# Performance work log

Hardware: AMD Instinct MI355X
Metric: run time of the kernel (lower is better)

Reference implementation:

```python
import jax, jax.numpy as jnp
from jax import lax
import numpy as np
import math

B, T, D = 4, 4096, 1024
K, H = 128, 8
KH = K // H
KER = 4
M = 4 * D  # mlp hidden


def _ln(x, g, b):
    m = jnp.mean(x, axis=-1, keepdims=True)
    v = jnp.var(x, axis=-1, keepdims=True)
    return (x - m) / jnp.sqrt(v + 1e-5) * g + b


def setup_inputs() -> dict:
    key = jax.random.key(0)
    ks = jax.random.split(key, 20)
    s = lambda i, shape, sc=0.02: jax.random.normal(ks[i], shape, dtype=jnp.float32) * sc
    inp = {}
    inp["x"] = jax.random.normal(ks[0], (B, T, D), dtype=jnp.float32)
    inp["prev_eig"] = jax.random.normal(ks[1], (B, T, 2 * K), dtype=jnp.float32)
    inp["in_proj_w"] = s(2, (2 * K, D))
    inp["conv_w"] = s(3, (2 * K, 1, KER), 0.3)          # depthwise Conv1d weight
    inp["conv_b"] = s(4, (2 * K,), 0.02)
    inp["mem_gate"] = jnp.float32(-3.0)
    inp["mem_proj_w"] = jnp.eye(2 * K, dtype=jnp.float32) + s(5, (2 * K, 2 * K), 0.02)
    # log_decay uniform in [center-1, center+0.5], center = -2 + 1.5*(1/5)
    center = -2.0 + 1.5 * (1.0 / 5.0)
    inp["log_decay"] = jax.random.uniform(ks[6], (K,), dtype=jnp.float32, minval=center - 1.0, maxval=center + 0.5)
    inp["frequency"] = jnp.linspace(0.0, 2.0 * math.pi * (1.0 - 1.0 / K), K, dtype=jnp.float32)
    inp["coupling"] = jnp.eye(KH, dtype=jnp.float32)[None] + 0.01 * jax.random.normal(ks[7], (H, KH, KH), dtype=jnp.float32) / math.sqrt(KH)
    inp["out_proj_w"] = s(8, (D, 2 * K))
    inp["gate_w"] = s(9, (D, D))
    inp["gate_b"] = jnp.full((D,), -2.0, dtype=jnp.float32)
    inp["mlp_w1"] = s(10, (M, D))
    inp["mlp_b1"] = jnp.zeros((M,), jnp.float32)
    inp["mlp_w2"] = s(11, (D, M))
    inp["mlp_b2"] = jnp.zeros((D,), jnp.float32)
    inp["n1_g"] = jnp.ones((D,), jnp.float32)
    inp["n1_b"] = jnp.zeros((D,), jnp.float32)
    inp["n2_g"] = jnp.ones((D,), jnp.float32)
    inp["n2_b"] = jnp.zeros((D,), jnp.float32)
    return inp


def reference(x, prev_eig, in_proj_w, conv_w, conv_b, mem_gate, mem_proj_w,
              log_decay, frequency, coupling, out_proj_w, gate_w, gate_b,
              mlp_w1, mlp_b1, mlp_w2, mlp_b2, n1_g, n1_b, n2_g, n2_b):
    Bn, Tn, Dn = x.shape
    xn = _ln(x, n1_g, n1_b)
    beta = xn @ in_proj_w.T                                   # [B,T,2K]
    # depthwise causal conv: torch pad=ker-1 both sides then [:, :, :T] == left-pad ker-1 + valid
    ker = conv_w.shape[-1]
    bp = jnp.pad(beta, ((0, 0), (ker - 1, 0), (0, 0))).transpose(0, 2, 1)  # [B,2K,T+ker-1]
    beta = lax.conv_general_dilated(bp, conv_w, (1,), 'VALID',
                                    feature_group_count=conv_w.shape[0],
                                    dimension_numbers=('NCH', 'OIH', 'NCH'))
    beta = jax.nn.silu(beta.transpose(0, 2, 1) + conv_b)       # [B,T,2K]
    br, bi = jnp.split(beta, 2, axis=-1)                       # [B,T,K] each
    # memory injection (has_memory: layer_idx > 0)
    mg = jax.nn.sigmoid(mem_gate)
    pr, pi = jnp.split(prev_eig @ mem_proj_w.T, 2, axis=-1)
    br = br + mg * pr
    bi = bi + mg * pi
    # eigenstate evolution via zero-padded complex FFT convolution
    mag = jax.nn.sigmoid(log_decay)                            # [K]
    n = jnp.arange(Tn, dtype=x.dtype)
    mag_pow = mag[None, :] ** n[:, None]                       # [T,K]
    phase = n[:, None] * frequency[None, :]
    kern = mag_pow * (jnp.cos(phase) + 1j * jnp.sin(phase))    # complex [T,K]
    beta_c = br + 1j * bi
    Bf = jnp.fft.fft(jnp.pad(beta_c, ((0, 0), (0, Tn), (0, 0))), axis=1)  # [B,2T,K]
    Kf = jnp.fft.fft(jnp.pad(kern, ((0, Tn), (0, 0))), axis=0)            # [2T,K]
    c = jnp.fft.ifft(Bf * Kf[None], axis=1)[:, :Tn]
    cr, ci = c.real.astype(x.dtype), c.imag.astype(x.dtype)
    # per-head coupling, batched over heads
    Hh, Kh = coupling.shape[0], coupling.shape[1]
    cr = jnp.einsum('hjk,bthk->bthj', coupling, cr.reshape(Bn, Tn, Hh, Kh)).reshape(Bn, Tn, Hh * Kh)
    ci = jnp.einsum('hjk,bthk->bthj', coupling, ci.reshape(Bn, Tn, Hh, Kh)).reshape(Bn, Tn, Hh * Kh)
    eig = jnp.concatenate([cr, ci], axis=-1)                   # [B,T,2K]
    h = jax.nn.sigmoid(xn @ gate_w.T + gate_b) * (eig @ out_proj_w.T)
    x1 = x + h
    y = _ln(x1, n2_g, n2_b)
    x2 = x1 + jax.nn.silu(y @ mlp_w1.T + mlp_b1) @ mlp_w2.T + mlp_b2
    return (x2, eig)
```

## Files before the change

### kernel.cpp

```cpp
#include <hip/hip_runtime.h>
#include <hip/hip_bf16.h>
#include <math.h>

#define Bn 4
#define Tn 4096
#define Dn 1024
#define Kn 128
#define TWOK 256
#define Hn 8
#define Mmlp 4096
#define NROW (Bn * Tn)
#define TAPS 16

typedef __attribute__((ext_vector_type(8))) short bf16x8;
typedef __attribute__((ext_vector_type(4))) float floatx4;

__device__ __forceinline__ float sigmoidf_(float x) { return 1.f / (1.f + expf(-x)); }

__global__ __launch_bounds__(256) void f2bf_kernel(const float* __restrict__ in,
                                                   __hip_bfloat16* __restrict__ out,
                                                   int n) {
    const int i = (blockIdx.x * 256 + threadIdx.x) * 4;
    if (i >= n) return;
    const float4 v = *(const float4*)(in + i);
    out[i + 0] = __float2bfloat16(v.x);
    out[i + 1] = __float2bfloat16(v.y);
    out[i + 2] = __float2bfloat16(v.z);
    out[i + 3] = __float2bfloat16(v.w);
}

__global__ __launch_bounds__(256) void ln_kernel(const float* __restrict__ x,
                                                 const float* __restrict__ g,
                                                 const float* __restrict__ b,
                                                 __hip_bfloat16* __restrict__ out) {
    const int row = blockIdx.x;
    const float4* xr = (const float4*)(x + (size_t)row * Dn);
    float4 v = xr[threadIdx.x];
    float s = v.x + v.y + v.z + v.w;
    float ss = v.x * v.x + v.y * v.y + v.z * v.z + v.w * v.w;
    for (int off = 32; off; off >>= 1) {
        s += __shfl_down(s, off);
        ss += __shfl_down(ss, off);
    }
    __shared__ float rs[4], rss[4];
    const int wv = threadIdx.x >> 6, ln = threadIdx.x & 63;
    if (ln == 0) { rs[wv] = s; rss[wv] = ss; }
    __syncthreads();
    s = rs[0] + rs[1] + rs[2] + rs[3];
    ss = rss[0] + rss[1] + rss[2] + rss[3];
    const float mean = s * (1.f / Dn);
    const float var = ss * (1.f / Dn) - mean * mean;
    const float inv = rsqrtf(var + 1e-5f);
    const float4 gg = ((const float4*)g)[threadIdx.x];
    const float4 bb = ((const float4*)b)[threadIdx.x];
    __hip_bfloat16* op = out + (size_t)row * Dn + threadIdx.x * 4;
    op[0] = __float2bfloat16((v.x - mean) * inv * gg.x + bb.x);
    op[1] = __float2bfloat16((v.y - mean) * inv * gg.y + bb.y);
    op[2] = __float2bfloat16((v.z - mean) * inv * gg.z + bb.z);
    op[3] = __float2bfloat16((v.w - mean) * inv * gg.w + bb.w);
}

template <int EPI, typename CT>
__global__ __launch_bounds__(256, 4) void gemm_bf(const ushort* __restrict__ A,
                                                  const ushort* __restrict__ B,
                                                  CT* __restrict__ C,
                                                  int M, int N, int Kd,
                                                  const float* __restrict__ bias,
                                                  const float* __restrict__ aux1,
                                                  const __hip_bfloat16* __restrict__ aux2) {
    __shared__ ushort As[128 * 32];
    __shared__ ushort Bs[128 * 32];
    const int tid = threadIdx.x;
    const int m0 = blockIdx.y * 128, n0 = blockIdx.x * 128;
    const int wave = tid >> 6, lane = tid & 63;
    const int wm = wave >> 1, wn = wave & 1;
    const int mlane = lane & 15, quad = lane >> 4;

    floatx4 acc[4][4] = {};

    const ushort* Ap = A + (size_t)m0 * Kd;
    const ushort* Bp = B + (size_t)n0 * Kd;

    for (int k0 = 0; k0 < Kd; k0 += 32) {
#pragma unroll
        for (int q = 0; q < 2; ++q) {
            const int c = q * 256 + tid;
            const int row = c >> 2, kc = (c & 3) * 8;
            __builtin_amdgcn_global_load_lds(
                (const __attribute__((address_space(1))) void*)(Ap + (size_t)row * Kd + k0 + kc),
                (__attribute__((address_space(3))) void*)(As + c * 8), 16, 0, 0);
            __builtin_amdgcn_global_load_lds(
                (const __attribute__((address_space(1))) void*)(Bp + (size_t)row * Kd + k0 + kc),
                (__attribute__((address_space(3))) void*)(Bs + c * 8), 16, 0, 0);
        }
        __syncthreads();

        bf16x8 af[4], bfr[4];
#pragma unroll
        for (int t = 0; t < 4; ++t) {
            af[t]  = *(const bf16x8*)&As[(wm * 64 + t * 16 + mlane) * 32 + quad * 8];
            bfr[t] = *(const bf16x8*)&Bs[(wn * 64 + t * 16 + mlane) * 32 + quad * 8];
        }
#pragma unroll
        for (int i = 0; i < 4; ++i)
#pragma unroll
            for (int j = 0; j < 4; ++j)
                acc[i][j] = __builtin_amdgcn_mfma_f32_16x16x32_bf16(af[i], bfr[j], acc[i][j], 0, 0, 0);
        __syncthreads();
    }

    float s_pre = 0.f;
    if constexpr (EPI == 1) s_pre = sigmoidf_(bias[0]);

    const int cbase = n0 + wn * 64 + mlane;
#pragma unroll
    for (int i = 0; i < 4; ++i) {
#pragma unroll
        for (int r = 0; r < 4; ++r) {
            const int row = m0 + wm * 64 + i * 16 + quad * 4 + r;
            const size_t ro = (size_t)row * N;
#pragma unroll
            for (int j = 0; j < 4; ++j) {
                const int col = cbase + j * 16;
                const float a = acc[i][j][r];
                float o;
                if constexpr (EPI == 0) {
                    o = a;
                } else if constexpr (EPI == 1) {
                    o = s_pre * a;
                } else if constexpr (EPI == 2) {
                    o = aux1[ro + col] + sigmoidf_(a + bias[col]) * __bfloat162float(aux2[ro + col]);
                } else if constexpr (EPI == 3) {
                    const float t = a + bias[col];
                    o = t * sigmoidf_(t);
                } else {
                    o = a + bias[col] + aux1[ro + col];
                }
                if constexpr (__is_same(CT, float)) C[ro + col] = o;
                else                                C[ro + col] = __float2bfloat16(o);
            }
        }
    }
}

#define TCH 256
#define BROWS (TCH + TAPS + 2)
#define UROWS (TCH + TAPS - 1)

__global__ __launch_bounds__(256) void cfc_kernel(const float* __restrict__ beta,
                                                  const float* __restrict__ mgp,
                                                  const float* __restrict__ conv_w,
                                                  const float* __restrict__ conv_b,
                                                  const float* __restrict__ log_decay,
                                                  const float* __restrict__ freq,
                                                  const float* __restrict__ coup,
                                                  float* __restrict__ eig,
                                                  __hip_bfloat16* __restrict__ eig_bf) {
    const int b = blockIdx.z, h = blockIdx.y, t0 = blockIdx.x * TCH;
    const int tid = threadIdx.x;

    __shared__ float sbeta[BROWS * 32];
    __shared__ float su[UROWS * 33];
    __shared__ float str[16 * TAPS], sti[16 * TAPS];
    __shared__ float scoup[16 * 16];
    __shared__ float scw[32 * 4], scb[32];

    auto chan = [&](int cg) { return (cg < 16) ? (h * 16 + cg) : (128 + h * 16 + cg - 16); };

    for (int idx = tid; idx < BROWS * 32; idx += 256) {
        const int r = idx >> 5, cg = idx & 31;
        const int t = t0 - (TAPS + 2) + r;
        sbeta[idx] = (t >= 0) ? beta[((size_t)b * Tn + t) * TWOK + chan(cg)] : 0.f;
    }
    for (int idx = tid; idx < UROWS * 32; idx += 256) {
        const int r = idx >> 5, cg = idx & 31;
        const int t = t0 - (TAPS - 1) + r;
        su[r * 33 + cg] = (t >= 0) ? mgp[((size_t)b * Tn + t) * TWOK + chan(cg)] : 0.f;
    }
    if (tid < 128) scw[tid] = conv_w[chan(tid >> 2) * 4 + (tid & 3)];
    else if (tid < 160) scb[tid - 128] = conv_b[chan(tid - 128)];
    scoup[tid] = coup[h * 256 + tid];
    {
        const int k = tid >> 4, d = tid & (TAPS - 1);
        const float mag = sigmoidf_(log_decay[h * 16 + k]);
        const float f = freq[h * 16 + k];
        const float p = powf(mag, (float)d);
        str[k * TAPS + d] = p * cosf(d * f);
        sti[k * TAPS + d] = p * sinf(d * f);
    }
    __syncthreads();

    for (int idx = tid; idx < UROWS * 32; idx += 256) {
        const int r = idx >> 5, cg = idx & 31;
        const int rb = r + 3;
        float v = sbeta[(rb - 3) * 32 + cg] * scw[cg * 4 + 0] +
                  sbeta[(rb - 2) * 32 + cg] * scw[cg * 4 + 1] +
                  sbeta[(rb - 1) * 32 + cg] * scw[cg * 4 + 2] +
                  sbeta[(rb - 0) * 32 + cg] * scw[cg * 4 + 3] + scb[cg];
        v = v * sigmoidf_(v);
        su[r * 33 + cg] += v;
    }
    __syncthreads();

    const int ru = tid + (TAPS - 1);
    float orr[16], oii[16];
#pragma unroll
    for (int j = 0; j < 16; ++j) { orr[j] = 0.f; oii[j] = 0.f; }
#pragma unroll 4
    for (int k = 0; k < 16; ++k) {
        float accr = 0.f, acci = 0.f;
#pragma unroll
        for (int d = 0; d < TAPS; ++d) {
            const float ur = su[(ru - d) * 33 + k];
            const float ui = su[(ru - d) * 33 + 16 + k];
            const float lr = str[k * TAPS + d], li = sti[k * TAPS + d];
            accr += lr * ur - li * ui;
            acci += lr * ui + li * ur;
        }
#pragma unroll
        for (int j = 0; j < 16; ++j) {
            orr[j] += scoup[j * 16 + k] * accr;
            oii[j] += scoup[j * 16 + k] * acci;
        }
    }
    const size_t base = ((size_t)b * Tn + t0 + tid) * TWOK + h * 16;
    float4* er = (float4*)(eig + base);
    float4* ei = (float4*)(eig + base + Kn);
#pragma unroll
    for (int q = 0; q < 4; ++q) {
        er[q] = make_float4(orr[4 * q], orr[4 * q + 1], orr[4 * q + 2], orr[4 * q + 3]);
        ei[q] = make_float4(oii[4 * q], oii[4 * q + 1], oii[4 * q + 2], oii[4 * q + 3]);
    }
#pragma unroll
    for (int j = 0; j < 16; ++j) {
        eig_bf[base + j] = __float2bfloat16(orr[j]);
        eig_bf[base + Kn + j] = __float2bfloat16(oii[j]);
    }
}

extern "C" void kernel_launch(void* const* d_in, const int* in_sizes, int n_in,
                              void* d_out, int out_size, void* d_ws, size_t ws_size,
                              hipStream_t stream) {
    const float* x          = (const float*)d_in[0];
    const float* prev_eig   = (const float*)d_in[1];
    const float* in_proj_w  = (const float*)d_in[2];
    const float* conv_w     = (const float*)d_in[3];
    const float* conv_b     = (const float*)d_in[4];
    const float* mem_gate   = (const float*)d_in[5];
    const float* mem_proj_w = (const float*)d_in[6];
    const float* log_decay  = (const float*)d_in[7];
    const float* frequency  = (const float*)d_in[8];
    const float* coupling   = (const float*)d_in[9];
    const float* out_proj_w = (const float*)d_in[10];
    const float* gate_w     = (const float*)d_in[11];
    const float* gate_b     = (const float*)d_in[12];
    const float* mlp_w1     = (const float*)d_in[13];
    const float* mlp_b1     = (const float*)d_in[14];
    const float* mlp_w2     = (const float*)d_in[15];
    const float* mlp_b2     = (const float*)d_in[16];
    const float* n1_g       = (const float*)d_in[17];
    const float* n1_b       = (const float*)d_in[18];
    const float* n2_g       = (const float*)d_in[19];
    const float* n2_b       = (const float*)d_in[20];

    float* out = (float*)d_out;
    float* eig = out + (size_t)NROW * Dn;

    char* wsb = (char*)d_ws;
    const size_t MB = 1 << 20;
    float* x1    = (float*)(wsb + 0);
    float* beta  = (float*)(wsb + 0);
    float* mgp   = (float*)(wsb + 16 * MB);
    __hip_bfloat16* h1      = (__hip_bfloat16*)(wsb + 64 * MB);
    __hip_bfloat16* o_bf    = (__hip_bfloat16*)(wsb + 64 * MB);
    __hip_bfloat16* eig_bf  = (__hip_bfloat16*)(wsb + 96 * MB);
    __hip_bfloat16* peig_bf = (__hip_bfloat16*)(wsb + 104 * MB);
    __hip_bfloat16* xn_bf   = (__hip_bfloat16*)(wsb + 128 * MB);
    __hip_bfloat16* y_bf    = (__hip_bfloat16*)(wsb + 160 * MB);
    __hip_bfloat16* w1_bf   = (__hip_bfloat16*)(wsb + 192 * MB);
    __hip_bfloat16* w2_bf   = (__hip_bfloat16*)(wsb + 200 * MB);
    __hip_bfloat16* gate_bf = (__hip_bfloat16*)(wsb + 208 * MB);
    __hip_bfloat16* inpj_bf = (__hip_bfloat16*)(wsb + 210 * MB);
    __hip_bfloat16* outpj_bf= (__hip_bfloat16*)(wsb + 210 * MB + 512 * 1024);
    __hip_bfloat16* mempj_bf= (__hip_bfloat16*)(wsb + 211 * MB);

    auto cvt = [&](const float* src, __hip_bfloat16* dst, int n) {
        f2bf_kernel<<<dim3((n / 4 + 255) / 256), dim3(256), 0, stream>>>(src, dst, n);
    };
    cvt(in_proj_w,  inpj_bf,  TWOK * Dn);
    cvt(mem_proj_w, mempj_bf, TWOK * TWOK);
    cvt(out_proj_w, outpj_bf, Dn * TWOK);
    cvt(gate_w,     gate_bf,  Dn * Dn);
    cvt(mlp_w1,     w1_bf,    Mmlp * Dn);
    cvt(mlp_w2,     w2_bf,    Dn * Mmlp);
    cvt(prev_eig,   peig_bf,  NROW * TWOK);

    ln_kernel<<<dim3(NROW), dim3(256), 0, stream>>>(x, n1_g, n1_b, xn_bf);
    gemm_bf<0, float><<<dim3(2, 128), dim3(256), 0, stream>>>(
        (const ushort*)xn_bf, (const ushort*)inpj_bf, beta, NROW, TWOK, Dn,
        nullptr, nullptr, nullptr);
    gemm_bf<1, float><<<dim3(2, 128), dim3(256), 0, stream>>>(
        (const ushort*)peig_bf, (const ushort*)mempj_bf, mgp, NROW, TWOK, TWOK,
        mem_gate, nullptr, nullptr);
    cfc_kernel<<<dim3(Tn / TCH, Hn, Bn), dim3(256), 0, stream>>>(
        beta, mgp, conv_w, conv_b, log_decay, frequency, coupling, eig, eig_bf);
    gemm_bf<0, __hip_bfloat16><<<dim3(8, 128), dim3(256), 0, stream>>>(
        (const ushort*)eig_bf, (const ushort*)outpj_bf, o_bf, NROW, Dn, TWOK,
        nullptr, nullptr, nullptr);
    gemm_bf<2, float><<<dim3(8, 128), dim3(256), 0, stream>>>(
        (const ushort*)xn_bf, (const ushort*)gate_bf, x1, NROW, Dn, Dn,
        gate_b, x, o_bf);
    ln_kernel<<<dim3(NROW), dim3(256), 0, stream>>>(x1, n2_g, n2_b, y_bf);
    for (int ck = 0; ck < 2; ++ck) {
        const size_t roff = (size_t)ck * 8192 * Dn;
        gemm_bf<3, __hip_bfloat16><<<dim3(32, 64), dim3(256), 0, stream>>>(
            (const ushort*)(y_bf + roff), (const ushort*)w1_bf, h1, 8192, Mmlp, Dn,
            mlp_b1, nullptr, nullptr);
        gemm_bf<4, float><<<dim3(8, 64), dim3(256), 0, stream>>>(
            (const ushort*)h1, (const ushort*)w2_bf, out + roff, 8192, Dn, Mmlp,
            mlp_b2, x1 + roff, nullptr);
    }
}
```

Before: 809.1 us.

## Fuse out_proj GEMM into gate GEMM epilogue and add XCD block swizzle

Computes eig·out_projᵀ as a second accumulator inside the gate GEMM kernel, so the bf16 o intermediate and its separate launch are no longer needed. The fused kernel keeps two accumulator sets and lowers occupancy to 2 blocks per CU. It also remaps block IDs across 8 groups for all GEMMs, changing tile-to-XCD assignment and cache locality. The fused epilogue now uses the fp32 product directly rather than a bf16-rounded one.

```diff
diff --git a/kernel.cpp b/kernel.cpp
--- a/kernel.cpp
+++ b/kernel.cpp
@@ -61,52 +61,91 @@
 }
 
 template <int EPI, typename CT>
-__global__ __launch_bounds__(256, 4) void gemm_bf(const ushort* __restrict__ A,
-                                                  const ushort* __restrict__ B,
-                                                  CT* __restrict__ C,
-                                                  int M, int N, int Kd,
-                                                  const float* __restrict__ bias,
-                                                  const float* __restrict__ aux1,
-                                                  const __hip_bfloat16* __restrict__ aux2) {
+__global__ __launch_bounds__(256, EPI == 5 ? 2 : 4)
+void gemm_bf(const ushort* __restrict__ A,
+             const ushort* __restrict__ B,
+             CT* __restrict__ C,
+             int M, int N, int Kd,
+             const float* __restrict__ bias,
+             const float* __restrict__ aux1,
+             const __hip_bfloat16* __restrict__ aux2,
+             const ushort* __restrict__ A2, const ushort* __restrict__ B2, int Kd2) {
     __shared__ ushort As[128 * 32];
     __shared__ ushort Bs[128 * 32];
     const int tid = threadIdx.x;
-    const int m0 = blockIdx.y * 128, n0 = blockIdx.x * 128;
+    const int nbx = gridDim.x;
+    const int nblk = nbx * gridDim.y;
+    int bid = blockIdx.y * nbx + blockIdx.x;
+    if ((nblk & 7) == 0)
+        bid = (bid & 7) * (nblk >> 3) + (bid >> 3);
+    const int m0 = (bid / nbx) * 128, n0 = (bid % nbx) * 128;
     const int wave = tid >> 6, lane = tid & 63;
     const int wm = wave >> 1, wn = wave & 1;
     const int mlane = lane & 15, quad = lane >> 4;
 
     floatx4 acc[4][4] = {};
 
-    const ushort* Ap = A + (size_t)m0 * Kd;
-    const ushort* Bp = B + (size_t)n0 * Kd;
-
-    for (int k0 = 0; k0 < Kd; k0 += 32) {
-#pragma unroll
-        for (int q = 0; q < 2; ++q) {
-            const int c = q * 256 + tid;
-            const int row = c >> 2, kc = (c & 3) * 8;
-            __builtin_amdgcn_global_load_lds(
-                (const __attribute__((address_space(1))) void*)(Ap + (size_t)row * Kd + k0 + kc),
-                (__attribute__((address_space(3))) void*)(As + c * 8), 16, 0, 0);
-            __builtin_amdgcn_global_load_lds(
-                (const __attribute__((address_space(1))) void*)(Bp + (size_t)row * Kd + k0 + kc),
-                (__attribute__((address_space(3))) void*)(Bs + c * 8), 16, 0, 0);
-        }
-        __syncthreads();
-
-        bf16x8 af[4], bfr[4];
-#pragma unroll
-        for (int t = 0; t < 4; ++t) {
-            af[t]  = *(const bf16x8*)&As[(wm * 64 + t * 16 + mlane) * 32 + quad * 8];
-            bfr[t] = *(const bf16x8*)&Bs[(wn * 64 + t * 16 + mlane) * 32 + quad * 8];
-        }
-#pragma unroll
-        for (int i = 0; i < 4; ++i)
-#pragma unroll
-            for (int j = 0; j < 4; ++j)
-                acc[i][j] = __builtin_amdgcn_mfma_f32_16x16x32_bf16(af[i], bfr[j], acc[i][j], 0, 0, 0);
-        __syncthreads();
+    {
+        const ushort* Ap = A + (size_t)m0 * Kd;
+        const ushort* Bp = B + (size_t)n0 * Kd;
+        for (int k0 = 0; k0 < Kd; k0 += 32) {
+#pragma unroll
+            for (int q = 0; q < 2; ++q) {
+                const int c = q * 256 + tid;
+                const int row = c >> 2, kc = (c & 3) * 8;
+                __builtin_amdgcn_global_load_lds(
+                    (const __attribute__((address_space(1))) void*)(Ap + (size_t)row * Kd + k0 + kc),
+                    (__attribute__((address_space(3))) void*)(As + c * 8), 16, 0, 0);
+                __builtin_amdgcn_global_load_lds(
+                    (const __attribute__((address_space(1))) void*)(Bp + (size_t)row * Kd + k0 + kc),
+                    (__attribute__((address_space(3))) void*)(Bs + c * 8), 16, 0, 0);
+            }
+            __syncthreads();
+            bf16x8 af[4], bfr[4];
+#pragma unroll
+            for (int t = 0; t < 4; ++t) {
+                af[t]  = *(const bf16x8*)&As[(wm * 64 + t * 16 + mlane) * 32 + quad * 8];
+                bfr[t] = *(const bf16x8*)&Bs[(wn * 64 + t * 16 + mlane) * 32 + quad * 8];
+            }
+#pragma unroll
+            for (int i = 0; i < 4; ++i)
+#pragma unroll
+                for (int j = 0; j < 4; ++j)
+                    acc[i][j] = __builtin_amdgcn_mfma_f32_16x16x32_bf16(af[i], bfr[j], acc[i][j], 0, 0, 0);
+            __syncthreads();
+        }
+    }
+
+    floatx4 acc2[EPI == 5 ? 4 : 1][EPI == 5 ? 4 : 1] = {};
+    if constexpr (EPI == 5) {
+        const ushort* Ap = A2 + (size_t)m0 * Kd2;
+        const ushort* Bp = B2 + (size_t)n0 * Kd2;
+        for (int k0 = 0; k0 < Kd2; k0 += 32) {
+#pragma unroll
+            for (int q = 0; q < 2; ++q) {
+                const int c = q * 256 + tid;
+                const int row = c >> 2, kc = (c & 3) * 8;
+                __builtin_amdgcn_global_load_lds(
+                    (const __attribute__((address_space(1))) void*)(Ap + (size_t)row * Kd2 + k0 + kc),
+                    (__attribute__((address_space(3))) void*)(As + c * 8), 16, 0, 0);
+                __builtin_amdgcn_global_load_lds(
+                    (const __attribute__((address_space(1))) void*)(Bp + (size_t)row * Kd2 + k0 + kc),
+                    (__attribute__((address_space(3))) void*)(Bs + c * 8), 16, 0, 0);
+            }
+            __syncthreads();
+            bf16x8 af[4], bfr[4];
+#pragma unroll
+            for (int t = 0; t < 4; ++t) {
+                af[t]  = *(const bf16x8*)&As[(wm * 64 + t * 16 + mlane) * 32 + quad * 8];
+                bfr[t] = *(const bf16x8*)&Bs[(wn * 64 + t * 16 + mlane) * 32 + quad * 8];
+            }
+#pragma unroll
+            for (int i = 0; i < 4; ++i)
+#pragma unroll
+                for (int j = 0; j < 4; ++j)
+                    acc2[i][j] = __builtin_amdgcn_mfma_f32_16x16x32_bf16(af[i], bfr[j], acc2[i][j], 0, 0, 0);
+            __syncthreads();
+        }
     }
 
     float s_pre = 0.f;
@@ -133,8 +172,10 @@
                 } else if constexpr (EPI == 3) {
                     const float t = a + bias[col];
                     o = t * sigmoidf_(t);
+                } else if constexpr (EPI == 4) {
+                    o = a + bias[col] + aux1[ro + col];
                 } else {
-                    o = a + bias[col] + aux1[ro + col];
+                    o = aux1[ro + col] + sigmoidf_(a + bias[col]) * acc2[i][j][r];
                 }
                 if constexpr (__is_same(CT, float)) C[ro + col] = o;
                 else                                C[ro + col] = __float2bfloat16(o);
@@ -272,7 +313,6 @@
     float* beta  = (float*)(wsb + 0);
     float* mgp   = (float*)(wsb + 16 * MB);
     __hip_bfloat16* h1      = (__hip_bfloat16*)(wsb + 64 * MB);
-    __hip_bfloat16* o_bf    = (__hip_bfloat16*)(wsb + 64 * MB);
     __hip_bfloat16* eig_bf  = (__hip_bfloat16*)(wsb + 96 * MB);
     __hip_bfloat16* peig_bf = (__hip_bfloat16*)(wsb + 104 * MB);
     __hip_bfloat16* xn_bf   = (__hip_bfloat16*)(wsb + 128 * MB);
@@ -298,26 +338,23 @@
     ln_kernel<<<dim3(NROW), dim3(256), 0, stream>>>(x, n1_g, n1_b, xn_bf);
     gemm_bf<0, float><<<dim3(2, 128), dim3(256), 0, stream>>>(
         (const ushort*)xn_bf, (const ushort*)inpj_bf, beta, NROW, TWOK, Dn,
-        nullptr, nullptr, nullptr);
+        nullptr, nullptr, nullptr, nullptr, nullptr, 0);
     gemm_bf<1, float><<<dim3(2, 128), dim3(256), 0, stream>>>(
         (const ushort*)peig_bf, (const ushort*)mempj_bf, mgp, NROW, TWOK, TWOK,
-        mem_gate, nullptr, nullptr);
+        mem_gate, nullptr, nullptr, nullptr, nullptr, 0);
     cfc_kernel<<<dim3(Tn / TCH, Hn, Bn), dim3(256), 0, stream>>>(
         beta, mgp, conv_w, conv_b, log_decay, frequency, coupling, eig, eig_bf);
-    gemm_bf<0, __hip_bfloat16><<<dim3(8, 128), dim3(256), 0, stream>>>(
-        (const ushort*)eig_bf, (const ushort*)outpj_bf, o_bf, NROW, Dn, TWOK,
-        nullptr, nullptr, nullptr);
-    gemm_bf<2, float><<<dim3(8, 128), dim3(256), 0, stream>>>(
+    gemm_bf<5, float><<<dim3(8, 128), dim3(256), 0, stream>>>(
         (const ushort*)xn_bf, (const ushort*)gate_bf, x1, NROW, Dn, Dn,
-        gate_b, x, o_bf);
+        gate_b, x, nullptr, (const ushort*)eig_bf, (const ushort*)outpj_bf, TWOK);
     ln_kernel<<<dim3(NROW), dim3(256), 0, stream>>>(x1, n2_g, n2_b, y_bf);
     for (int ck = 0; ck < 2; ++ck) {
         const size_t roff = (size_t)ck * 8192 * Dn;
         gemm_bf<3, __hip_bfloat16><<<dim3(32, 64), dim3(256), 0, stream>>>(
             (const ushort*)(y_bf + roff), (const ushort*)w1_bf, h1, 8192, Mmlp, Dn,
-            mlp_b1, nullptr, nullptr);
+            mlp_b1, nullptr, nullptr, nullptr, nullptr, 0);
         gemm_bf<4, float><<<dim3(8, 64), dim3(256), 0, stream>>>(
             (const ushort*)h1, (const ushort*)w2_bf, out + roff, 8192, Dn, Mmlp,
-            mlp_b2, x1 + roff, nullptr);
-    }
-}
+            mlp_b2, x1 + roff, nullptr, nullptr, nullptr, 0);
+    }
+}
```

Result: faster. 785.4 us (-2.9%).
